# Kernel tuning notes

Measured on AMD Instinct MI355X. Metric: run time of the kernel, lower is better.

Reference implementation:

```python
import jax, jax.numpy as jnp
import numpy as np

G, T, S, M = 128, 512, 24, 4


def setup_inputs() -> dict:
    key = jax.random.key(0)
    k0, k1, k2, k3, k4 = jax.random.split(key, 5)
    inp = jax.random.normal(k0, (G, T, M), dtype=jnp.float32)
    # Stable-ish transition matrices: near 0.95*I
    F = 0.95 * jnp.eye(S, dtype=jnp.float32) + 0.05 * jax.random.normal(k1, (G, T, S, S), dtype=jnp.float32) / jnp.sqrt(S)
    # PSD process noise Q = c*A A^T + eps*I
    Aq = jax.random.normal(k2, (G, T, S, S), dtype=jnp.float32)
    Q = (0.01 / S) * jnp.einsum('gtik,gtjk->gtij', Aq, Aq) + 1e-3 * jnp.eye(S, dtype=jnp.float32)
    H = 0.5 * jax.random.normal(k3, (G, T, M, S), dtype=jnp.float32)
    # PSD measurement noise R
    Ar = jax.random.normal(k4, (G, T, M, M), dtype=jnp.float32)
    R = (0.1 / M) * jnp.einsum('gtik,gtjk->gtij', Ar, Ar) + 1e-2 * jnp.eye(M, dtype=jnp.float32)
    init_mean = jnp.zeros((G, S), dtype=jnp.float32)
    init_cov = jnp.broadcast_to(jnp.eye(S, dtype=jnp.float32), (G, S, S))
    return dict(input=inp, F=F, Q=Q, H=H, R=R, init_mean=init_mean, init_cov=init_cov)


def _measure(m, P, Hc, Rc):
    # one-step-ahead measurement distribution: mu = H m, Sig = H P H^T + R
    mu = jnp.einsum('gms,gs->gm', Hc, m)
    Sig = Hc @ P @ Hc.swapaxes(-1, -2) + Rc
    return mu, Sig


def _kalman(input, F, Q, H, R, init_mean, init_cov):
    # time-major for scan
    y = jnp.moveaxis(input, 1, 0)      # [T,G,M]
    Ft = jnp.moveaxis(F, 1, 0)         # [T,G,S,S]
    Qt = jnp.moveaxis(Q, 1, 0)
    Ht = jnp.moveaxis(H, 1, 0)         # [T,G,M,S]
    Rt = jnp.moveaxis(R, 1, 0)         # [T,G,M,M]

    mu0, Sig0 = _measure(init_mean, init_cov, Ht[0], Rt[0])

    def step(carry, x):
        m, P = carry                     # state prediction for t-1: [G,S], [G,S,S]
        yprev, Fp, Qp, Hp, Rp, Hc, Rc = x
        # --- update with obs at t-1 (using H,R from the t-1 measurement) ---
        HP = Hp @ P                      # [G,M,S]
        Sm = HP @ Hp.swapaxes(-1, -2) + Rp   # innovation cov [G,M,M]
        # K = P H^T S^{-1}; using symmetry: K = solve(S, H P)^T
        K = jnp.linalg.solve(Sm, HP).swapaxes(-1, -2)  # [G,S,M]
        resid = yprev - jnp.einsum('gms,gs->gm', Hp, m)
        m_u = m + jnp.einsum('gsm,gm->gs', K, resid)
        P_u = P - K @ HP
        # --- predict to t ---
        m_p = jnp.einsum('gij,gj->gi', Fp, m_u)
        P_p = Fp @ P_u @ Fp.swapaxes(-1, -2) + Qp
        # --- measurement at t ---
        mu, Sig = _measure(m_p, P_p, Hc, Rc)
        return (m_p, P_p), (mu, Sig)

    xs = (y[:-1], Ft[:-1], Qt[:-1], Ht[:-1], Rt[:-1], Ht[1:], Rt[1:])
    _, (mus, Sigs) = jax.lax.scan(step, (init_mean, init_cov), xs)
    means = jnp.moveaxis(jnp.concatenate([mu0[None], mus], axis=0), 0, 1)   # [G,T,M]
    covs = jnp.moveaxis(jnp.concatenate([Sig0[None], Sigs], axis=0), 0, 1)  # [G,T,M,M]
    return means, covs


def reference(input, F, Q, H, R, init_mean, init_cov):
    return _kalman(input, F, Q, H, R, init_mean, init_cov)
```

## Files before the change

kernel.cpp:

```cpp
#include <hip/hip_runtime.h>

#define Gn 128
#define Tn 512
#define Sn 24
#define SP 28
#define Mn 4
#define COVS_BASE (Gn * Tn * Mn)

__device__ __forceinline__ float4 ld4(const float* p) {
    return *reinterpret_cast<const float4*>(p);
}
__device__ __forceinline__ void st4(float* p, float4 v) {
    *reinterpret_cast<float4*>(p) = v;
}
__device__ __forceinline__ float dot4(float4 a, float4 b) {
    return a.x*b.x + a.y*b.y + a.z*b.z + a.w*b.w;
}

struct Row24 { float4 v[6]; };

__device__ __forceinline__ Row24 loadRow(const float* p) {
    Row24 r;
#pragma unroll
    for (int i = 0; i < 6; ++i) r.v[i] = ld4(p + 4*i);
    return r;
}

__device__ __forceinline__ float dot24(const Row24& a, const float* b) {
    float4 b0 = ld4(b+0), b1 = ld4(b+4), b2 = ld4(b+8),
           b3 = ld4(b+12), b4 = ld4(b+16), b5 = ld4(b+20);
    float s0 = a.v[0].x*b0.x + a.v[0].y*b0.y + a.v[0].z*b0.z + a.v[0].w*b0.w;
    float s1 = a.v[1].x*b1.x + a.v[1].y*b1.y + a.v[1].z*b1.z + a.v[1].w*b1.w;
    float s2 = a.v[2].x*b2.x + a.v[2].y*b2.y + a.v[2].z*b2.z + a.v[2].w*b2.w;
    float s3 = a.v[3].x*b3.x + a.v[3].y*b3.y + a.v[3].z*b3.z + a.v[3].w*b3.w;
    float s4 = a.v[4].x*b4.x + a.v[4].y*b4.y + a.v[4].z*b4.z + a.v[4].w*b4.w;
    float s5 = a.v[5].x*b5.x + a.v[5].y*b5.y + a.v[5].z*b5.z + a.v[5].w*b5.w;
    return ((s0+s1)+(s2+s3))+(s4+s5);
}

__device__ __forceinline__ void barrierLds() {
    asm volatile("s_waitcnt lgkmcnt(0)" ::: "memory");
    __builtin_amdgcn_s_barrier();
    asm volatile("" ::: "memory");
}
__device__ __forceinline__ void waveLds() {
    asm volatile("s_waitcnt lgkmcnt(0)" ::: "memory");
    __builtin_amdgcn_wave_barrier();
    asm volatile("" ::: "memory");
}

extern "C" __global__ void __launch_bounds__(256)
kalman_kernel(const float* __restrict__ y_g, const float* __restrict__ F_g,
              const float* __restrict__ Q_g, const float* __restrict__ H_g,
              const float* __restrict__ R_g, const float* __restrict__ m0_g,
              const float* __restrict__ P0_g, float* __restrict__ out)
{
    const int g   = blockIdx.x;
    const int tid = threadIdx.x;
    const int gT  = g * Tn;

    __shared__ __align__(16) float sP[Sn*SP];
    __shared__ __align__(16) float sPu[Sn*SP];
    __shared__ __align__(16) float sTmp[Sn*SP];
    __shared__ __align__(16) float sF[2][Sn*SP];
    __shared__ __align__(16) float sQ[2][Sn*SP];
    __shared__ __align__(16) float sH[2][Mn*SP];
    __shared__ __align__(16) float sR[2][16];
    __shared__ __align__(16) float sy[2][4];
    __shared__ __align__(16) float sHP[Mn*SP];
    __shared__ __align__(16) float sHPT[Sn*4];
    __shared__ __align__(16) float sK[Sn*4];
    __shared__ __align__(16) float sSig[16];
    __shared__ __align__(16) float sInv[16];
    __shared__ __align__(16) float sMean[Sn];
    __shared__ __align__(16) float sMu_[Sn];
    __shared__ __align__(16) float sResid[4];

    const float4* F4 = reinterpret_cast<const float4*>(F_g);
    const float4* Q4 = reinterpret_cast<const float4*>(Q_g);
    const float4* H4 = reinterpret_cast<const float4*>(H_g);
    const float4* R4 = reinterpret_cast<const float4*>(R_g);
    const float4* y4 = reinterpret_cast<const float4*>(y_g);

    auto stage_load = [&](int v, int t) -> float4 {
        if (v < 144)      return F4[(gT + t)*144 + v];
        else if (v < 288) return Q4[(gT + t)*144 + (v-144)];
        else if (v < 312) return H4[(gT + t)*24  + (v-288)];
        else if (v < 316) return R4[(gT + t)*4   + (v-312)];
        else              return y4[gT + t];
    };
    auto stage_store = [&](int v, int bb, float4 val) {
        if (v < 144)      { int r = v/6,        c = (v%6)*4;       st4(&sF[bb][r*SP+c], val); }
        else if (v < 288) { int v2 = v-144; int r = v2/6, c = (v2%6)*4; st4(&sQ[bb][r*SP+c], val); }
        else if (v < 312) { int v2 = v-288; int r = v2/6, c = (v2%6)*4; st4(&sH[bb][r*SP+c], val); }
        else if (v < 316) { st4(&sR[bb][(v-312)*4], val); }
        else              { st4(&sy[bb][0], val); }
    };

    if (tid < 144) {
        int r = tid / 6, c = (tid % 6) * 4;
        st4(&sP[r*SP + c], ld4(&P0_g[g*Sn*Sn + tid*4]));
    } else if (tid < 150) {
        int v = tid - 144;
        st4(&sMean[v*4], ld4(&m0_g[g*Sn + v*4]));
    }
    {
        float4 a0 = stage_load(tid, 0);
        stage_store(tid, 0, a0);
        if (tid + 256 < 317) {
            float4 a1 = stage_load(tid + 256, 0);
            stage_store(tid + 256, 0, a1);
        }
    }
    barrierLds();

    float4 pf0, pf1;

    for (int t = 0; t < Tn; ++t) {
        const int  b    = t & 1;
        const int  b1   = b ^ 1;
        const bool last = (t == Tn - 1);

        if (!last) {
            pf0 = stage_load(tid, t+1);
            if (tid + 256 < 317) pf1 = stage_load(tid + 256, t+1);
        }
        if (tid < 96) {
            int a = tid / 24, s = tid % 24;
            Row24 hr = loadRow(&sH[b][a*SP]);
            float hp = dot24(hr, &sP[s*SP]);
            sHP[a*SP + s]  = hp;
            sHPT[s*4 + a]  = hp;
        } else if (tid >= 128 && tid < 132) {
            int a = tid - 128;
            Row24 hr = loadRow(&sH[b][a*SP]);
            float mu = dot24(hr, sMean);
            out[(gT + t)*4 + a] = mu;
            sResid[a] = sy[b][a] - mu;
        }
        barrierLds();

        if (tid < 64) {
            if (tid < 16) {
                int a = tid >> 2, c = tid & 3;
                Row24 hpr = loadRow(&sHP[a*SP]);
                float sig = dot24(hpr, &sH[b][c*SP]) + sR[b][tid];
                sSig[tid] = sig;
                out[COVS_BASE + (size_t)(gT + t)*16 + tid] = sig;
            }
            if (!last) {
                waveLds();
                if (tid < 16) {
                    float s00=sSig[0],  s01=sSig[1],  s02=sSig[2],  s03=sSig[3];
                    float s10=sSig[4],  s11=sSig[5],  s12=sSig[6],  s13=sSig[7];
                    float s20=sSig[8],  s21=sSig[9],  s22=sSig[10], s23=sSig[11];
                    float s30=sSig[12], s31=sSig[13], s32=sSig[14], s33=sSig[15];
                    float p0 = s00*s11 - s01*s10;
                    float p1 = s00*s12 - s02*s10;
                    float p2 = s00*s13 - s03*s10;
                    float p3 = s01*s12 - s02*s11;
                    float p4 = s01*s13 - s03*s11;
                    float p5 = s02*s13 - s03*s12;
                    float q0c = s20*s31 - s21*s30;
                    float q1c = s20*s32 - s22*s30;
                    float q2c = s20*s33 - s23*s30;
                    float q3c = s21*s32 - s22*s31;
                    float q4c = s21*s33 - s23*s31;
                    float q5c = s22*s33 - s23*s32;
                    float det  = p0*q5c - p1*q4c + p2*q3c + p3*q2c - p4*q1c + p5*q0c;
                    float rdet = 1.0f / det;
                    int ia = tid >> 2, ic = tid & 3;
                    int r0 = (ic==0)?1:0, r1 = (ic<=1)?2:1, r2 = (ic<=2)?3:2;
                    int u0 = (ia==0)?1:0, u1 = (ia<=1)?2:1, u2 = (ia<=2)?3:2;
                    float m00=sSig[r0*4+u0], m01=sSig[r0*4+u1], m02=sSig[r0*4+u2];
                    float m10=sSig[r1*4+u0], m11=sSig[r1*4+u1], m12=sSig[r1*4+u2];
                    float m20=sSig[r2*4+u0], m21=sSig[r2*4+u1], m22=sSig[r2*4+u2];
                    float minor = m00*(m11*m22 - m12*m21)
                                - m01*(m10*m22 - m12*m20)
                                + m02*(m10*m21 - m11*m20);
                    float cof = ((ia + ic) & 1) ? -minor : minor;
                    sInv[tid] = cof * rdet;
                }
                waveLds();
                {
                    int a = tid / 24, s = tid % 24;
                    float kt = dot4(ld4(&sInv[a*4]), ld4(&sHPT[s*4]));
                    sK[s*4 + a] = kt;
                    if (tid < 32) {
                        int o2 = 64 + tid, a3 = o2/24, s3 = o2%24;
                        float kt2 = dot4(ld4(&sInv[a3*4]), ld4(&sHPT[s3*4]));
                        sK[s3*4 + a3] = kt2;
                    }
                }
            }
        }
        if (last) return;
        barrierLds();

        {
            int o = 2*tid, i = o/24, j = o%24;
            float4 kr = ld4(&sK[i*4]);
            float pu0 = sP[i*SP+j]   - dot4(kr, ld4(&sHPT[j*4]));
            float pu1 = sP[i*SP+j+1] - dot4(kr, ld4(&sHPT[(j+1)*4]));
            sPu[i*SP+j]   = pu0;
            sPu[i*SP+j+1] = pu1;
            if (tid >= 64 && tid < 128) {
                int o2 = 512 + (tid-64), i2 = o2/24, j2 = o2%24;
                sPu[i2*SP+j2] = sP[i2*SP+j2] - dot4(ld4(&sK[i2*4]), ld4(&sHPT[j2*4]));
            }
            if (tid >= 192 && tid < 216) {
                int s = tid - 192;
                sMu_[s] = sMean[s] + dot4(ld4(&sK[s*4]), ld4(&sResid[0]));
            }
        }
        barrierLds();

        {
            int o = 2*tid, i = o/24, j = o%24;
            Row24 fr = loadRow(&sF[b][i*SP]);
            sTmp[i*SP+j]   = dot24(fr, &sPu[j*SP]);
            sTmp[i*SP+j+1] = dot24(fr, &sPu[(j+1)*SP]);
            if (tid >= 64 && tid < 128) {
                int o2 = 512 + (tid-64), i2 = o2/24, j2 = o2%24;
                Row24 fr2 = loadRow(&sF[b][i2*SP]);
                sTmp[i2*SP+j2] = dot24(fr2, &sPu[j2*SP]);
            }
            if (tid >= 224 && tid < 248) {
                int i3 = tid - 224;
                Row24 fr3 = loadRow(&sF[b][i3*SP]);
                sMean[i3] = dot24(fr3, sMu_);
            }
        }
        barrierLds();

        {
            int o = 2*tid, i = o/24, j = o%24;
            Row24 tr = loadRow(&sTmp[i*SP]);
            sP[i*SP+j]   = dot24(tr, &sF[b][j*SP])     + sQ[b][i*SP+j];
            sP[i*SP+j+1] = dot24(tr, &sF[b][(j+1)*SP]) + sQ[b][i*SP+j+1];
            if (tid >= 64 && tid < 128) {
                int o2 = 512 + (tid-64), i2 = o2/24, j2 = o2%24;
                Row24 tr2 = loadRow(&sTmp[i2*SP]);
                sP[i2*SP+j2] = dot24(tr2, &sF[b][j2*SP]) + sQ[b][i2*SP+j2];
            }
            stage_store(tid, b1, pf0);
            if (tid + 256 < 317) stage_store(tid + 256, b1, pf1);
        }
        barrierLds();
    }
}

extern "C" void kernel_launch(void* const* d_in, const int* in_sizes, int n_in,
                              void* d_out, int out_size, void* d_ws, size_t ws_size,
                              hipStream_t stream) {
    kalman_kernel<<<Gn, 256, 0, stream>>>(
        (const float*)d_in[0], (const float*)d_in[1], (const float*)d_in[2],
        (const float*)d_in[3], (const float*)d_in[4], (const float*)d_in[5],
        (const float*)d_in[6], (float*)d_out);
}
```

Measured before the change: 1.283 ms.

## Reformulate update as F P F^T minus W S^-1 W^T with wave-specialized stages

Rewrites the covariance update algebraically: instead of computing P_u = P - K H P and then F P_u F^T, it computes FP = F P, W = FP H^T, and P_next = FP F^T + Q - W S^{-1} W^T, with the mean handled likewise. Work is split across the four waves (FP, mean, HP, Sigma and inverse) so the independent pieces run concurrently, which cuts the per-step barriers from five to three. Each lane computes a 3x3 register tile. The cost is that only one wave does the large 24x24 matmuls, so the per-step critical path through that wave may grow, and the rearranged arithmetic changes rounding.

```diff
diff --git a/kernel.cpp b/kernel.cpp
--- a/kernel.cpp
+++ b/kernel.cpp
@@ -29,12 +29,22 @@
 __device__ __forceinline__ float dot24(const Row24& a, const float* b) {
     float4 b0 = ld4(b+0), b1 = ld4(b+4), b2 = ld4(b+8),
            b3 = ld4(b+12), b4 = ld4(b+16), b5 = ld4(b+20);
-    float s0 = a.v[0].x*b0.x + a.v[0].y*b0.y + a.v[0].z*b0.z + a.v[0].w*b0.w;
-    float s1 = a.v[1].x*b1.x + a.v[1].y*b1.y + a.v[1].z*b1.z + a.v[1].w*b1.w;
-    float s2 = a.v[2].x*b2.x + a.v[2].y*b2.y + a.v[2].z*b2.z + a.v[2].w*b2.w;
-    float s3 = a.v[3].x*b3.x + a.v[3].y*b3.y + a.v[3].z*b3.z + a.v[3].w*b3.w;
-    float s4 = a.v[4].x*b4.x + a.v[4].y*b4.y + a.v[4].z*b4.z + a.v[4].w*b4.w;
-    float s5 = a.v[5].x*b5.x + a.v[5].y*b5.y + a.v[5].z*b5.z + a.v[5].w*b5.w;
+    float s0 = dot4(a.v[0], b0);
+    float s1 = dot4(a.v[1], b1);
+    float s2 = dot4(a.v[2], b2);
+    float s3 = dot4(a.v[3], b3);
+    float s4 = dot4(a.v[4], b4);
+    float s5 = dot4(a.v[5], b5);
+    return ((s0+s1)+(s2+s3))+(s4+s5);
+}
+
+__device__ __forceinline__ float dot24rr(const Row24& a, const Row24& b) {
+    float s0 = dot4(a.v[0], b.v[0]);
+    float s1 = dot4(a.v[1], b.v[1]);
+    float s2 = dot4(a.v[2], b.v[2]);
+    float s3 = dot4(a.v[3], b.v[3]);
+    float s4 = dot4(a.v[4], b.v[4]);
+    float s5 = dot4(a.v[5], b.v[5]);
     return ((s0+s1)+(s2+s3))+(s4+s5);
 }
 
@@ -60,20 +70,18 @@
     const int gT  = g * Tn;
 
     __shared__ __align__(16) float sP[Sn*SP];
-    __shared__ __align__(16) float sPu[Sn*SP];
-    __shared__ __align__(16) float sTmp[Sn*SP];
+    __shared__ __align__(16) float sFP[Sn*SP];
     __shared__ __align__(16) float sF[2][Sn*SP];
     __shared__ __align__(16) float sQ[2][Sn*SP];
     __shared__ __align__(16) float sH[2][Mn*SP];
     __shared__ __align__(16) float sR[2][16];
     __shared__ __align__(16) float sy[2][4];
     __shared__ __align__(16) float sHP[Mn*SP];
-    __shared__ __align__(16) float sHPT[Sn*4];
-    __shared__ __align__(16) float sK[Sn*4];
+    __shared__ __align__(16) float sW[Sn*4];
     __shared__ __align__(16) float sSig[16];
     __shared__ __align__(16) float sInv[16];
     __shared__ __align__(16) float sMean[Sn];
-    __shared__ __align__(16) float sMu_[Sn];
+    __shared__ __align__(16) float sFm[Sn];
     __shared__ __align__(16) float sResid[4];
 
     const float4* F4 = reinterpret_cast<const float4*>(F_g);
@@ -114,6 +122,14 @@
     }
     barrierLds();
 
+    const int w    = tid >> 6;
+    const int lane = tid & 63;
+    const int ib   = lane >> 3, jb = lane & 7;
+    const int i0   = 3*ib, j0 = 3*jb;
+    const int a2   = lane / 24,        s2 = lane % 24;
+    const int a3   = (64+lane) / 24,   s3 = (64+lane) % 24;
+    const int iW   = lane >> 1,        aW = (lane & 1) * 2;
+
     float4 pf0, pf1;
 
     for (int t = 0; t < Tn; ++t) {
@@ -125,32 +141,73 @@
             pf0 = stage_load(tid, t+1);
             if (tid + 256 < 317) pf1 = stage_load(tid + 256, t+1);
         }
-        if (tid < 96) {
-            int a = tid / 24, s = tid % 24;
-            Row24 hr = loadRow(&sH[b][a*SP]);
-            float hp = dot24(hr, &sP[s*SP]);
-            sHP[a*SP + s]  = hp;
-            sHPT[s*4 + a]  = hp;
-        } else if (tid >= 128 && tid < 132) {
-            int a = tid - 128;
-            Row24 hr = loadRow(&sH[b][a*SP]);
-            float mu = dot24(hr, sMean);
-            out[(gT + t)*4 + a] = mu;
-            sResid[a] = sy[b][a] - mu;
+
+        if (w == 0) {
+            if (!last) {
+                Row24 p0r = loadRow(&sP[(j0+0)*SP]);
+                Row24 p1r = loadRow(&sP[(j0+1)*SP]);
+                Row24 p2r = loadRow(&sP[(j0+2)*SP]);
+#pragma unroll
+                for (int r = 0; r < 3; ++r) {
+                    Row24 fr = loadRow(&sF[b][(i0+r)*SP]);
+                    sFP[(i0+r)*SP + j0+0] = dot24rr(fr, p0r);
+                    sFP[(i0+r)*SP + j0+1] = dot24rr(fr, p1r);
+                    sFP[(i0+r)*SP + j0+2] = dot24rr(fr, p2r);
+                }
+            }
+        } else if (w == 1) {
+            if (lane < 24 && !last) {
+                Row24 fr = loadRow(&sF[b][lane*SP]);
+                sFm[lane] = dot24(fr, sMean);
+            }
+        } else if (w == 2) {
+            Row24 hr = loadRow(&sH[b][a2*SP]);
+            sHP[a2*SP + s2] = dot24(hr, &sP[s2*SP]);
+        } else {
+            if (lane < 32) {
+                Row24 hr = loadRow(&sH[b][a3*SP]);
+                sHP[a3*SP + s3] = dot24(hr, &sP[s3*SP]);
+            } else if (lane < 36) {
+                int a = lane - 32;
+                Row24 hr = loadRow(&sH[b][a*SP]);
+                float mu = dot24(hr, sMean);
+                out[(gT + t)*4 + a] = mu;
+                sResid[a] = sy[b][a] - mu;
+            }
         }
         barrierLds();
 
-        if (tid < 64) {
-            if (tid < 16) {
-                int a = tid >> 2, c = tid & 3;
-                Row24 hpr = loadRow(&sHP[a*SP]);
-                float sig = dot24(hpr, &sH[b][c*SP]) + sR[b][tid];
-                sSig[tid] = sig;
-                out[COVS_BASE + (size_t)(gT + t)*16 + tid] = sig;
+        float acc[3][3];
+        if (w == 1) {
+            if (!last) {
+                Row24 fr0 = loadRow(&sF[b][(j0+0)*SP]);
+                Row24 fr1 = loadRow(&sF[b][(j0+1)*SP]);
+                Row24 fr2 = loadRow(&sF[b][(j0+2)*SP]);
+#pragma unroll
+                for (int r = 0; r < 3; ++r) {
+                    Row24 fp = loadRow(&sFP[(i0+r)*SP]);
+                    acc[r][0] = dot24rr(fp, fr0);
+                    acc[r][1] = dot24rr(fp, fr1);
+                    acc[r][2] = dot24rr(fp, fr2);
+                }
+            }
+        } else if (w == 2) {
+            if (lane < 48 && !last) {
+                Row24 fp = loadRow(&sFP[iW*SP]);
+                sW[iW*4 + aW]     = dot24(fp, &sH[b][aW*SP]);
+                sW[iW*4 + aW + 1] = dot24(fp, &sH[b][(aW+1)*SP]);
+            }
+        } else if (w == 3) {
+            if (lane < 16) {
+                int a = lane >> 2, bb = lane & 3;
+                Row24 hp = loadRow(&sHP[a*SP]);
+                float sig = dot24(hp, &sH[b][bb*SP]) + sR[b][lane];
+                sSig[lane] = sig;
+                out[COVS_BASE + (size_t)(gT + t)*16 + lane] = sig;
             }
             if (!last) {
                 waveLds();
-                if (tid < 16) {
+                if (lane < 16) {
                     float s00=sSig[0],  s01=sSig[1],  s02=sSig[2],  s03=sSig[3];
                     float s10=sSig[4],  s11=sSig[5],  s12=sSig[6],  s13=sSig[7];
                     float s20=sSig[8],  s21=sSig[9],  s22=sSig[10], s23=sSig[11];
@@ -169,7 +226,7 @@
                     float q5c = s22*s33 - s23*s32;
                     float det  = p0*q5c - p1*q4c + p2*q3c + p3*q2c - p4*q1c + p5*q0c;
                     float rdet = 1.0f / det;
-                    int ia = tid >> 2, ic = tid & 3;
+                    int ia = lane >> 2, ic = lane & 3;
                     int r0 = (ic==0)?1:0, r1 = (ic<=1)?2:1, r2 = (ic<=2)?3:2;
                     int u0 = (ia==0)?1:0, u1 = (ia<=1)?2:1, u2 = (ia<=2)?3:2;
                     float m00=sSig[r0*4+u0], m01=sSig[r0*4+u1], m02=sSig[r0*4+u2];
@@ -179,73 +236,40 @@
                                 - m01*(m10*m22 - m12*m20)
                                 + m02*(m10*m21 - m11*m20);
                     float cof = ((ia + ic) & 1) ? -minor : minor;
-                    sInv[tid] = cof * rdet;
-                }
-                waveLds();
-                {
-                    int a = tid / 24, s = tid % 24;
-                    float kt = dot4(ld4(&sInv[a*4]), ld4(&sHPT[s*4]));
-                    sK[s*4 + a] = kt;
-                    if (tid < 32) {
-                        int o2 = 64 + tid, a3 = o2/24, s3 = o2%24;
-                        float kt2 = dot4(ld4(&sInv[a3*4]), ld4(&sHPT[s3*4]));
-                        sK[s3*4 + a3] = kt2;
-                    }
+                    sInv[lane] = cof * rdet;
                 }
             }
         }
         if (last) return;
         barrierLds();
 
-        {
-            int o = 2*tid, i = o/24, j = o%24;
-            float4 kr = ld4(&sK[i*4]);
-            float pu0 = sP[i*SP+j]   - dot4(kr, ld4(&sHPT[j*4]));
-            float pu1 = sP[i*SP+j+1] - dot4(kr, ld4(&sHPT[(j+1)*4]));
-            sPu[i*SP+j]   = pu0;
-            sPu[i*SP+j+1] = pu1;
-            if (tid >= 64 && tid < 128) {
-                int o2 = 512 + (tid-64), i2 = o2/24, j2 = o2%24;
-                sPu[i2*SP+j2] = sP[i2*SP+j2] - dot4(ld4(&sK[i2*4]), ld4(&sHPT[j2*4]));
-            }
-            if (tid >= 192 && tid < 216) {
-                int s = tid - 192;
-                sMu_[s] = sMean[s] + dot4(ld4(&sK[s*4]), ld4(&sResid[0]));
-            }
-        }
-        barrierLds();
-
-        {
-            int o = 2*tid, i = o/24, j = o%24;
-            Row24 fr = loadRow(&sF[b][i*SP]);
-            sTmp[i*SP+j]   = dot24(fr, &sPu[j*SP]);
-            sTmp[i*SP+j+1] = dot24(fr, &sPu[(j+1)*SP]);
-            if (tid >= 64 && tid < 128) {
-                int o2 = 512 + (tid-64), i2 = o2/24, j2 = o2%24;
-                Row24 fr2 = loadRow(&sF[b][i2*SP]);
-                sTmp[i2*SP+j2] = dot24(fr2, &sPu[j2*SP]);
-            }
-            if (tid >= 224 && tid < 248) {
-                int i3 = tid - 224;
-                Row24 fr3 = loadRow(&sF[b][i3*SP]);
-                sMean[i3] = dot24(fr3, sMu_);
-            }
-        }
-        barrierLds();
-
-        {
-            int o = 2*tid, i = o/24, j = o%24;
-            Row24 tr = loadRow(&sTmp[i*SP]);
-            sP[i*SP+j]   = dot24(tr, &sF[b][j*SP])     + sQ[b][i*SP+j];
-            sP[i*SP+j+1] = dot24(tr, &sF[b][(j+1)*SP]) + sQ[b][i*SP+j+1];
-            if (tid >= 64 && tid < 128) {
-                int o2 = 512 + (tid-64), i2 = o2/24, j2 = o2%24;
-                Row24 tr2 = loadRow(&sTmp[i2*SP]);
-                sP[i2*SP+j2] = dot24(tr2, &sF[b][j2*SP]) + sQ[b][i2*SP+j2];
-            }
-            stage_store(tid, b1, pf0);
-            if (tid + 256 < 317) stage_store(tid + 256, b1, pf1);
-        }
+        if (w == 1) {
+            float4 inv0 = ld4(&sInv[0]),  inv1 = ld4(&sInv[4]);
+            float4 inv2 = ld4(&sInv[8]),  inv3 = ld4(&sInv[12]);
+            float4 wj0 = ld4(&sW[(j0+0)*4]);
+            float4 wj1 = ld4(&sW[(j0+1)*4]);
+            float4 wj2 = ld4(&sW[(j0+2)*4]);
+#pragma unroll
+            for (int r = 0; r < 3; ++r) {
+                float4 wi = ld4(&sW[(i0+r)*4]);
+                float4 X  = make_float4(dot4(wi,inv0), dot4(wi,inv1),
+                                        dot4(wi,inv2), dot4(wi,inv3));
+                sP[(i0+r)*SP + j0+0] = acc[r][0] + sQ[b][(i0+r)*SP + j0+0] - dot4(X, wj0);
+                sP[(i0+r)*SP + j0+1] = acc[r][1] + sQ[b][(i0+r)*SP + j0+1] - dot4(X, wj1);
+                sP[(i0+r)*SP + j0+2] = acc[r][2] + sQ[b][(i0+r)*SP + j0+2] - dot4(X, wj2);
+            }
+        } else if (w == 2) {
+            if (lane < 24) {
+                float4 inv0 = ld4(&sInv[0]),  inv1 = ld4(&sInv[4]);
+                float4 inv2 = ld4(&sInv[8]),  inv3 = ld4(&sInv[12]);
+                float4 ws = ld4(&sW[lane*4]);
+                float4 Xs = make_float4(dot4(ws,inv0), dot4(ws,inv1),
+                                        dot4(ws,inv2), dot4(ws,inv3));
+                sMean[lane] = sFm[lane] + dot4(Xs, ld4(&sResid[0]));
+            }
+        }
+        stage_store(tid, b1, pf0);
+        if (tid + 256 < 317) stage_store(tid + 256, b1, pf1);
         barrierLds();
     }
 }
```

Measured after the change: 1.316 ms. 2.6% more time.
